# Kernel tuning notes

Hardware: AMD Instinct MI355X
Metric: run time of the kernel (lower is better)

## Reference

```python
import jax, jax.numpy as jnp
import numpy as np

N = 100000
H = 8      # heads
C = 8      # out channels per head
NEG_SLOPE = 0.2
EPS = 1e-16


def setup_inputs() -> dict:
    key = jax.random.key(0)
    k1, k2, k3, k4, k5, k6 = jax.random.split(key, 6)
    x = jax.random.normal(k1, (N, 128), dtype=jnp.float32)
    edge_index = jax.random.randint(k2, (2, 1600000), 0, N, dtype=jnp.int64)
    W = jax.random.normal(k3, (128, H * C), dtype=jnp.float32) * (1.0 / np.sqrt(128))
    att_src = jax.random.normal(k4, (H, C), dtype=jnp.float32)
    att_dst = jax.random.normal(k5, (H, C), dtype=jnp.float32)
    bias = jax.random.normal(k6, (H * C,), dtype=jnp.float32) * 0.01
    return {"x": x, "edge_index": edge_index, "W": W,
            "att_src": att_src, "att_dst": att_dst, "bias": bias}


def _gat_forward(x, edge_index, W, att_src, att_dst, bias):
    # add self loops (PyG GATConv default add_self_loops=True)
    loop = jnp.arange(N, dtype=edge_index.dtype)
    src = jnp.concatenate([edge_index[0], loop])
    dst = jnp.concatenate([edge_index[1], loop])

    h = (x @ W).reshape(N, H, C)                       # [N,H,C]
    a_src = jnp.sum(h * att_src, axis=-1)              # [N,H]
    a_dst = jnp.sum(h * att_dst, axis=-1)              # [N,H]

    e = a_src[src] + a_dst[dst]                        # [E,H]
    e = jnp.where(e > 0, e, NEG_SLOPE * e)             # leaky_relu(0.2)

    # segment softmax over edges grouped by destination node
    m = jax.ops.segment_max(e, dst, num_segments=N)    # [N,H]
    m = jnp.where(jnp.isfinite(m), m, 0.0)
    ex = jnp.exp(e - m[dst])                           # [E,H]
    denom = jax.ops.segment_sum(ex, dst, num_segments=N)
    alpha = ex / (denom[dst] + EPS)                    # [E,H]

    msg = alpha[:, :, None] * h[src]                   # [E,H,C]
    out = jax.ops.segment_sum(msg, dst, num_segments=N)  # [N,H,C]
    out = out.reshape(N, H * C) + bias
    return jax.nn.relu(out)


def reference(x, edge_index, W, att_src, att_dst, bias):
    return _gat_forward(x, edge_index, W, att_src, att_dst, bias)
```

## Files before the change

kernel.cpp:

```cpp
#include <hip/hip_runtime.h>
#include <hip/hip_bf16.h>

#define NNODES 100000
#define NH 8
#define OUTD 64
#define FDIM 128
#define NEG_SLOPE 0.2f
#define NBUCK ((NNODES + 255) / 256)
#define MAXB 5376
#define CH 4096
#define ROWS_PB 128
#define NFB ((NNODES + ROWS_PB - 1) / ROWS_PB)
#define SHST 68

typedef __attribute__((ext_vector_type(8))) short bf16x8;
typedef __attribute__((ext_vector_type(4))) float f32x4;
typedef __attribute__((ext_vector_type(4))) unsigned int u32x4;

static __device__ __forceinline__ unsigned short f2bf(float f) {
    __hip_bfloat16 b = __float2bfloat16(f);
    return *(unsigned short*)&b;
}

__global__ void k_wprep(const float* __restrict__ W, unsigned short* __restrict__ wimg)
{
    int i = blockIdx.x * 256 + threadIdx.x;
    if (i >= FDIM * OUTD) return;
    int k = i >> 6, col = i & 63;
    int chs = (k >> 3) ^ (col & 15);
    wimg[col * FDIM + chs * 8 + (k & 7)] = f2bf(W[i]);
}

__global__ __launch_bounds__(256) void k_feat(
    const float* __restrict__ x, const unsigned short* __restrict__ wimg,
    const float* __restrict__ att_s, const float* __restrict__ att_d,
    __hip_bfloat16* __restrict__ h, float* __restrict__ asrc,
    float* __restrict__ adst)
{
    __shared__ unsigned short sx[ROWS_PB * FDIM];
    __shared__ unsigned short swt[OUTD * FDIM];
    __shared__ float shf[4 * 16 * SHST];
    __shared__ float sAs[OUTD], sAd[OUTD];

    int tid = threadIdx.x;
    if (tid < OUTD) { sAs[tid] = att_s[tid]; sAd[tid] = att_d[tid]; }

    {
        const u32x4* src = (const u32x4*)wimg;
        u32x4* dst = (u32x4*)swt;
        for (int i = tid; i < (OUTD * FDIM) / 8; i += 256) dst[i] = src[i];
    }
    int row0 = blockIdx.x * ROWS_PB;
    for (int c = tid; c < ROWS_PB * 16; c += 256) {
        int row = c >> 4, chunk = c & 15;
        int grow = row0 + row;
        unsigned short tmp[8];
        if (grow < NNODES) {
            const float* p = x + (size_t)grow * FDIM + chunk * 8;
            f32x4 f0 = *(const f32x4*)p;
            f32x4 f1 = *(const f32x4*)(p + 4);
#pragma unroll
            for (int j = 0; j < 4; ++j) tmp[j] = f2bf(f0[j]);
#pragma unroll
            for (int j = 0; j < 4; ++j) tmp[4 + j] = f2bf(f1[j]);
        } else {
#pragma unroll
            for (int j = 0; j < 8; ++j) tmp[j] = 0;
        }
        int chs = chunk ^ (row & 15);
        *(bf16x8*)&sx[row * FDIM + chs * 8] = *(bf16x8*)tmp;
    }
    __syncthreads();

    int w = tid >> 6, l = tid & 63;
    int l4 = l & 15, g = l >> 4;

    bf16x8 bfrag[16];
#pragma unroll
    for (int n = 0; n < 4; ++n)
#pragma unroll
        for (int kk = 0; kk < 4; ++kk) {
            int col = n * 16 + l4;
            int chs = (kk * 4 + g) ^ l4;
            bfrag[n * 4 + kk] = *(const bf16x8*)&swt[col * FDIM + chs * 8];
        }

    float* mysh = &shf[w * 16 * SHST];

#pragma unroll
    for (int rt = 0; rt < 2; ++rt) {
        int lbase = w * 32 + rt * 16;
        f32x4 acc[4];
#pragma unroll
        for (int n = 0; n < 4; ++n) acc[n] = (f32x4){0.f, 0.f, 0.f, 0.f};

#pragma unroll
        for (int kk = 0; kk < 4; ++kk) {
            int row = lbase + l4;
            int chs = (kk * 4 + g) ^ l4;
            bf16x8 a = *(const bf16x8*)&sx[row * FDIM + chs * 8];
#pragma unroll
            for (int n = 0; n < 4; ++n)
                acc[n] = __builtin_amdgcn_mfma_f32_16x16x32_bf16(
                    a, bfrag[n * 4 + kk], acc[n], 0, 0, 0);
        }

#pragma unroll
        for (int n = 0; n < 4; ++n)
#pragma unroll
            for (int r = 0; r < 4; ++r)
                mysh[(g * 4 + r) * SHST + n * 16 + l4] = acc[n][r];

#pragma unroll
        for (int i = 0; i < 2; ++i) {
            int c = i * 64 + l;
            int row = c >> 3, ch = c & 7;
            int grow = row0 + lbase + row;
            if (grow < NNODES) {
                const float* rp = &mysh[row * SHST + ch * 8];
                unsigned short tmp[8];
#pragma unroll
                for (int j = 0; j < 8; ++j) tmp[j] = f2bf(rp[j]);
                *(bf16x8*)&h[(size_t)grow * OUTD + ch * 8] = *(bf16x8*)tmp;
            }
        }
#pragma unroll
        for (int i = 0; i < 2; ++i) {
            int t = i * 64 + l;
            int row = t >> 3, hd = t & 7;
            int grow = row0 + lbase + row;
            if (grow < NNODES) {
                const float* rp = &mysh[row * SHST + hd * 8];
                float s1 = 0.f, s2 = 0.f;
#pragma unroll
                for (int j = 0; j < 8; ++j) {
                    s1 = fmaf(rp[j], sAs[hd * 8 + j], s1);
                    s2 = fmaf(rp[j], sAd[hd * 8 + j], s2);
                }
                asrc[grow * NH + hd] = s1;
                adst[grow * NH + hd] = s2;
            }
        }
    }
}

__global__ __launch_bounds__(256) void k_bin(
    const int* __restrict__ ei, int E, int* __restrict__ gCur,
    unsigned int* __restrict__ gSorted)
{
    __shared__ int cnt[NBUCK];
    __shared__ int base[NBUCK];
    int tot = E + NNODES;
    int e0 = blockIdx.x * CH;
    int e1 = e0 + CH; if (e1 > tot) e1 = tot;

    for (int i = threadIdx.x; i < NBUCK; i += 256) cnt[i] = 0;
    __syncthreads();

    for (int i = e0 + threadIdx.x; i < e1; i += 256) {
        int d = (i < E) ? ei[E + i] : (i - E);
        atomicAdd(&cnt[d >> 8], 1);
    }
    __syncthreads();

    for (int i = threadIdx.x; i < NBUCK; i += 256) {
        int c = cnt[i];
        base[i] = (c > 0) ? atomicAdd(&gCur[i], c) : 0;
        cnt[i] = 0;
    }
    __syncthreads();

    for (int i = e0 + threadIdx.x; i < e1; i += 256) {
        int s, d;
        if (i < E) { s = ei[i]; d = ei[E + i]; }
        else       { s = d = i - E; }
        int b = d >> 8;
        int p = base[b] + atomicAdd(&cnt[b], 1);
        if (p < MAXB)
            gSorted[(size_t)b * MAXB + p] =
                ((unsigned int)(d & 255) << 17) | (unsigned int)s;
    }
}

__global__ __launch_bounds__(256) void k_csr(
    const int* __restrict__ gCur, unsigned int* __restrict__ gSorted,
    int2* __restrict__ rows)
{
    __shared__ unsigned int ent[MAXB];
    __shared__ int cnt[256], scn[256], cur[256];
    int b = blockIdx.x;
    int n = gCur[b]; if (n > MAXB) n = MAXB;
    size_t gbase = (size_t)b * MAXB;

    for (int i = threadIdx.x; i < n; i += 256) ent[i] = gSorted[gbase + i];
    cnt[threadIdx.x] = 0;
    __syncthreads();

    for (int i = threadIdx.x; i < n; i += 256)
        atomicAdd(&cnt[ent[i] >> 17], 1);
    __syncthreads();

    int v = cnt[threadIdx.x];
    int acc = v;
    scn[threadIdx.x] = v;
    __syncthreads();
    for (int off = 1; off < 256; off <<= 1) {
        int t = (threadIdx.x >= (unsigned)off) ? scn[threadIdx.x - off] : 0;
        __syncthreads();
        acc += t;
        scn[threadIdx.x] = acc;
        __syncthreads();
    }
    int ex = acc - v;

    int node = (b << 8) + threadIdx.x;
    if (node < NNODES)
        rows[node] = make_int2((int)gbase + ex, (int)gbase + ex + v);
    cur[threadIdx.x] = ex;
    __syncthreads();

    for (int i = threadIdx.x; i < n; i += 256) {
        unsigned int p = ent[i];
        int pos = atomicAdd(&cur[p >> 17], 1);
        gSorted[gbase + pos] = p & 0x1FFFFu;
    }
}

__global__ __launch_bounds__(256) void k_gather(
    const int2* __restrict__ rows, const unsigned int* __restrict__ esrc,
    const __hip_bfloat16* __restrict__ h, const float* __restrict__ asrc,
    const float* __restrict__ adst, const float* __restrict__ bias,
    float* __restrict__ out)
{
    int node = (blockIdx.x * 256 + threadIdx.x) >> 6;
    if (node >= NNODES) return;
    int lane = threadIdx.x & 63;
    int l5 = lane >> 5;
    int c  = lane & 31;
    int hh = c >> 2;

    float adh = adst[(unsigned)(node * NH + hh)];
    int2 se = rows[node];
    int start = se.x, end = se.y;
    const unsigned* hu = (const unsigned*)h;

    float num0 = 0.f, num1 = 0.f, den = 0.f;

    for (int base = start; base < end; base += 64) {
        int cnt = end - base; if (cnt > 64) cnt = 64;
        int sj = (base + lane < end) ? (int)esrc[base + lane] : 0;

        auto pair = [&](int k) {
            int s2 = __shfl(sj, k + l5);
            float a = asrc[(unsigned)(s2 * NH + hh)];
            unsigned w = hu[(unsigned)(s2 * 32 + c)];
            float e = a + adh;
            e = fmaxf(e, NEG_SLOPE * e);
            float ex = __expf(e);
            den += ex;
            union { unsigned u; float f; } lo, hi;
            lo.u = w << 16; hi.u = w & 0xffff0000u;
            num0 = fmaf(ex, lo.f, num0);
            num1 = fmaf(ex, hi.f, num1);
        };

        int k = 0;
        for (; k + 4 <= cnt; k += 4) { pair(k); pair(k + 2); }
        for (; k + 2 <= cnt; k += 2) { pair(k); }
        if (k < cnt) {
            int s2 = __shfl(sj, k);
            float a = asrc[(unsigned)(s2 * NH + hh)];
            unsigned w = hu[(unsigned)(s2 * 32 + c)];
            float e = a + adh;
            e = fmaxf(e, NEG_SLOPE * e);
            float ex = l5 ? 0.f : __expf(e);
            den += ex;
            union { unsigned u; float f; } lo, hi;
            lo.u = w << 16; hi.u = w & 0xffff0000u;
            num0 = fmaf(ex, lo.f, num0);
            num1 = fmaf(ex, hi.f, num1);
        }
    }

    num0 += __shfl_xor(num0, 32);
    num1 += __shfl_xor(num1, 32);
    den  += __shfl_xor(den, 32);

    int ch = c * 2 + l5;
    float inv = 1.f / (den + 1e-16f);
    float vv = (l5 ? num1 : num0) * inv + bias[ch];
    out[(unsigned)(node * OUTD + ch)] = vv > 0.f ? vv : 0.f;
}

extern "C" void kernel_launch(void* const* d_in, const int* in_sizes, int n_in,
                              void* d_out, int out_size, void* d_ws, size_t ws_size,
                              hipStream_t stream)
{
    const float* x     = (const float*)d_in[0];
    const int*   ei    = (const int*)  d_in[1];
    const float* W     = (const float*)d_in[2];
    const float* att_s = (const float*)d_in[3];
    const float* att_d = (const float*)d_in[4];
    const float* bias  = (const float*)d_in[5];
    float* out = (float*)d_out;
    int E = in_sizes[1] / 2;
    int tot = E + NNODES;

    __hip_bfloat16* h = (__hip_bfloat16*)d_ws;
    float* asrc   = (float*)(h + (size_t)NNODES * OUTD);
    float* adst   = asrc + (size_t)NNODES * NH;
    int2*  rows   = (int2*)(adst + (size_t)NNODES * NH);
    int*   gCur   = (int*)(rows + NNODES);
    unsigned int* gSorted = (unsigned int*)(gCur + 512);
    unsigned short* wimg  = (unsigned short*)(gSorted + (size_t)NBUCK * MAXB);

    hipMemsetAsync(gCur, 0, 512 * sizeof(int), stream);

    k_wprep<<<(FDIM * OUTD + 255) / 256, 256, 0, stream>>>(W, wimg);
    k_feat<<<NFB, 256, 0, stream>>>(x, wimg, att_s, att_d, h, asrc, adst);
    k_bin<<<(tot + CH - 1) / CH, 256, 0, stream>>>(ei, E, gCur, gSorted);
    k_csr<<<NBUCK, 256, 0, stream>>>(gCur, gSorted, rows);
    k_gather<<<(NNODES * 64 + 255) / 256, 256, 0, stream>>>(
        rows, gSorted, h, asrc, adst, bias, out);
}
```

Baseline: 125.4 us.

## Partition node features by head and split gather across head-sliced blocks

Stores h, asrc and adst head-major (one contiguous slice per head), and restructures the gather so each block handles a single head for 8 nodes. Consecutive blocks cycle through the 8 heads, so each wave touches only one head's slice at a time. The aim is better L2 locality for the random source-node gathers, since each head slice is much smaller than the full feature table. In exchange, the edge index list is reloaded 8 times (once per head), more shuffle reductions are needed, and only a quarter of the lanes do the final stores.

```diff
diff --git a/kernel.cpp b/kernel.cpp
--- a/kernel.cpp
+++ b/kernel.cpp
@@ -34,8 +34,8 @@
 __global__ __launch_bounds__(256) void k_feat(
     const float* __restrict__ x, const unsigned short* __restrict__ wimg,
     const float* __restrict__ att_s, const float* __restrict__ att_d,
-    __hip_bfloat16* __restrict__ h, float* __restrict__ asrc,
-    float* __restrict__ adst)
+    unsigned short* __restrict__ hq, float* __restrict__ asrc_p,
+    float* __restrict__ adst_p)
 {
     __shared__ unsigned short sx[ROWS_PB * FDIM];
     __shared__ unsigned short swt[OUTD * FDIM];
@@ -121,7 +121,7 @@
                 unsigned short tmp[8];
 #pragma unroll
                 for (int j = 0; j < 8; ++j) tmp[j] = f2bf(rp[j]);
-                *(bf16x8*)&h[(size_t)grow * OUTD + ch * 8] = *(bf16x8*)tmp;
+                *(bf16x8*)&hq[((size_t)ch * NNODES + grow) * 8] = *(bf16x8*)tmp;
             }
         }
 #pragma unroll
@@ -137,8 +137,8 @@
                     s1 = fmaf(rp[j], sAs[hd * 8 + j], s1);
                     s2 = fmaf(rp[j], sAd[hd * 8 + j], s2);
                 }
-                asrc[grow * NH + hd] = s1;
-                adst[grow * NH + hd] = s2;
+                asrc_p[hd * NNODES + grow] = s1;
+                adst_p[hd * NNODES + grow] = s2;
             }
         }
     }
@@ -228,68 +228,60 @@
 
 __global__ __launch_bounds__(256) void k_gather(
     const int2* __restrict__ rows, const unsigned int* __restrict__ esrc,
-    const __hip_bfloat16* __restrict__ h, const float* __restrict__ asrc,
-    const float* __restrict__ adst, const float* __restrict__ bias,
+    const unsigned short* __restrict__ hq, const float* __restrict__ asrc_p,
+    const float* __restrict__ adst_p, const float* __restrict__ bias,
     float* __restrict__ out)
 {
-    int node = (blockIdx.x * 256 + threadIdx.x) >> 6;
-    if (node >= NNODES) return;
+    int q  = blockIdx.x & 7;
+    int bo = blockIdx.x >> 3;
+    int wv = threadIdx.x >> 6;
     int lane = threadIdx.x & 63;
-    int l5 = lane >> 5;
-    int c  = lane & 31;
-    int hh = c >> 2;
-
-    float adh = adst[(unsigned)(node * NH + hh)];
+    int half = lane >> 5;
+    int sub  = lane & 31;
+    int slot = sub >> 2;
+    int li   = sub & 3;
+
+    int node = bo * 8 + wv * 2 + half;
+
+    float adh = adst_p[q * NNODES + node];
     int2 se = rows[node];
-    int start = se.x, end = se.y;
-    const unsigned* hu = (const unsigned*)h;
-
-    float num0 = 0.f, num1 = 0.f, den = 0.f;
-
-    for (int base = start; base < end; base += 64) {
-        int cnt = end - base; if (cnt > 64) cnt = 64;
-        int sj = (base + lane < end) ? (int)esrc[base + lane] : 0;
-
-        auto pair = [&](int k) {
-            int s2 = __shfl(sj, k + l5);
-            float a = asrc[(unsigned)(s2 * NH + hh)];
-            unsigned w = hu[(unsigned)(s2 * 32 + c)];
+    const float* asp = asrc_p + q * NNODES;
+    const unsigned* hp = (const unsigned*)hq + (size_t)q * NNODES * 4;
+
+    float n0 = 0.f, n1 = 0.f, den = 0.f;
+    int pl = (lane & 32) + slot;
+
+    for (int base = se.x; base < se.y; base += 32) {
+        int cnt = se.y - base; if (cnt > 32) cnt = 32;
+        int sj = (sub < cnt) ? (int)esrc[base + sub] : 0;
+        for (int k = 0; k < cnt; k += 8) {
+            int s2 = __shfl(sj, pl + k);
+            bool valid = (k + slot) < cnt;
+            float a = asp[s2];
+            unsigned w = hp[(unsigned)(s2 * 4 + li)];
             float e = a + adh;
             e = fmaxf(e, NEG_SLOPE * e);
-            float ex = __expf(e);
+            float ex = valid ? __expf(e) : 0.f;
             den += ex;
             union { unsigned u; float f; } lo, hi;
             lo.u = w << 16; hi.u = w & 0xffff0000u;
-            num0 = fmaf(ex, lo.f, num0);
-            num1 = fmaf(ex, hi.f, num1);
-        };
-
-        int k = 0;
-        for (; k + 4 <= cnt; k += 4) { pair(k); pair(k + 2); }
-        for (; k + 2 <= cnt; k += 2) { pair(k); }
-        if (k < cnt) {
-            int s2 = __shfl(sj, k);
-            float a = asrc[(unsigned)(s2 * NH + hh)];
-            unsigned w = hu[(unsigned)(s2 * 32 + c)];
-            float e = a + adh;
-            e = fmaxf(e, NEG_SLOPE * e);
-            float ex = l5 ? 0.f : __expf(e);
-            den += ex;
-            union { unsigned u; float f; } lo, hi;
-            lo.u = w << 16; hi.u = w & 0xffff0000u;
-            num0 = fmaf(ex, lo.f, num0);
-            num1 = fmaf(ex, hi.f, num1);
-        }
-    }
-
-    num0 += __shfl_xor(num0, 32);
-    num1 += __shfl_xor(num1, 32);
-    den  += __shfl_xor(den, 32);
-
-    int ch = c * 2 + l5;
-    float inv = 1.f / (den + 1e-16f);
-    float vv = (l5 ? num1 : num0) * inv + bias[ch];
-    out[(unsigned)(node * OUTD + ch)] = vv > 0.f ? vv : 0.f;
+            n0 = fmaf(ex, lo.f, n0);
+            n1 = fmaf(ex, hi.f, n1);
+        }
+    }
+
+    n0 += __shfl_xor(n0, 4);  n0 += __shfl_xor(n0, 8);  n0 += __shfl_xor(n0, 16);
+    n1 += __shfl_xor(n1, 4);  n1 += __shfl_xor(n1, 8);  n1 += __shfl_xor(n1, 16);
+    den += __shfl_xor(den, 4); den += __shfl_xor(den, 8); den += __shfl_xor(den, 16);
+
+    if (slot == 0) {
+        float inv = 1.f / (den + 1e-16f);
+        int ch = q * 8 + li * 2;
+        float2 v;
+        v.x = fmaxf(n0 * inv + bias[ch], 0.f);
+        v.y = fmaxf(n1 * inv + bias[ch + 1], 0.f);
+        *(float2*)&out[(unsigned)(node * OUTD + ch)] = v;
+    }
 }
 
 extern "C" void kernel_launch(void* const* d_in, const int* in_sizes, int n_in,
@@ -306,10 +298,10 @@
     int E = in_sizes[1] / 2;
     int tot = E + NNODES;
 
-    __hip_bfloat16* h = (__hip_bfloat16*)d_ws;
-    float* asrc   = (float*)(h + (size_t)NNODES * OUTD);
-    float* adst   = asrc + (size_t)NNODES * NH;
-    int2*  rows   = (int2*)(adst + (size_t)NNODES * NH);
+    unsigned short* hq = (unsigned short*)d_ws;
+    float* asrc_p = (float*)(hq + (size_t)NNODES * OUTD);
+    float* adst_p = asrc_p + (size_t)NNODES * NH;
+    int2*  rows   = (int2*)(adst_p + (size_t)NNODES * NH);
     int*   gCur   = (int*)(rows + NNODES);
     unsigned int* gSorted = (unsigned int*)(gCur + 512);
     unsigned short* wimg  = (unsigned short*)(gSorted + (size_t)NBUCK * MAXB);
@@ -317,9 +309,9 @@
     hipMemsetAsync(gCur, 0, 512 * sizeof(int), stream);
 
     k_wprep<<<(FDIM * OUTD + 255) / 256, 256, 0, stream>>>(W, wimg);
-    k_feat<<<NFB, 256, 0, stream>>>(x, wimg, att_s, att_d, h, asrc, adst);
+    k_feat<<<NFB, 256, 0, stream>>>(x, wimg, att_s, att_d, hq, asrc_p, adst_p);
     k_bin<<<(tot + CH - 1) / CH, 256, 0, stream>>>(ei, E, gCur, gSorted);
     k_csr<<<NBUCK, 256, 0, stream>>>(gCur, gSorted, rows);
-    k_gather<<<(NNODES * 64 + 255) / 256, 256, 0, stream>>>(
-        rows, gSorted, h, asrc, adst, bias, out);
-}
+    k_gather<<<NNODES, 256, 0, stream>>>(
+        rows, gSorted, hq, asrc_p, adst_p, bias, out);
+}
```

New measurement: 201.1 us. 1.6x slower.
